# Kernel tuning notes

Hardware: AMD Instinct MI355X
Metric: run time of the kernel (lower is better)

Reference implementation:

```python
import jax, jax.numpy as jnp
import numpy as np

N_LOW = 50000
N_HIGH = 200000
E = 1000000       # number of (i, j, k) triplets from the radius search
K = 27            # 3x3x3 voxel kernel cells
C_IN = 128
C_OUT = 128


def setup_inputs() -> dict:
    key = jax.random.key(0)
    k0, k1, k2, k3, k4, k5 = jax.random.split(key, 6)
    x_low = jax.random.normal(k0, (N_LOW, C_IN), dtype=jnp.float32)
    # PointConv3d weight: one [C_OUT, C_IN] matrix per kernel cell, kaiming-ish scale
    weight = jax.random.normal(k1, (K, C_OUT, C_IN), dtype=jnp.float32) * (1.0 / np.sqrt(C_IN))
    bias = jax.random.normal(k2, (C_OUT,), dtype=jnp.float32) * 0.01
    i_high = jax.random.randint(k3, (E,), 0, N_HIGH, dtype=jnp.int32)
    j_low = jax.random.randint(k4, (E,), 0, N_LOW, dtype=jnp.int32)
    k_cell = jax.random.randint(k5, (E,), 0, K, dtype=jnp.int32)
    return {"x_low": x_low, "weight": weight, "bias": bias,
            "i_high": i_high, "j_low": j_low, "k": k_cell, "n_high": N_HIGH}


def reference(x_low, weight, bias, i_high, j_low, k, n_high):
    # Sparse point convolution: out[i] += weight[k] @ x_low[j], then + bias.
    # Efficient form: transform every low-res point by all K kernel matrices once
    # (dense GEMM), then gather the (j, k) entry per triplet and scatter-add by i.
    y = jnp.einsum('nc,koc->nko', x_low, weight)       # [N_low, K, C_out]
    msg = y[j_low, k]                                  # [E, C_out] gather
    out = jnp.zeros((n_high, weight.shape[1]), dtype=x_low.dtype)
    out = out.at[i_high].add(msg)                      # scatter-add to high-res points
    return out + bias
```

## Files before the change

kernel.cpp:

```cpp
#include <hip/hip_runtime.h>

typedef _Float16 half8 __attribute__((ext_vector_type(8)));
typedef _Float16 half4v __attribute__((ext_vector_type(4)));
typedef _Float16 half2v __attribute__((ext_vector_type(2)));
typedef float f32x4 __attribute__((ext_vector_type(4)));
typedef float f32x2 __attribute__((ext_vector_type(2)));

#define CAP 32
#define OVF_MAX 4096


__global__ void init_bias(float* __restrict__ out, const float* __restrict__ bias, int n4) {
    int i = blockIdx.x * blockDim.x + threadIdx.x;
    if (i >= n4) return;
    reinterpret_cast<float4*>(out)[i] = reinterpret_cast<const float4*>(bias)[i & 31];
}

__global__ __launch_bounds__(256) void cvt_mask(
    const float* __restrict__ x, const float* __restrict__ w,
    const float* __restrict__ bias,
    _Float16* __restrict__ Xh, _Float16* __restrict__ Wh,
    float* __restrict__ biasPerm, _Float16* __restrict__ Yz,
    const int* __restrict__ ih, const int* __restrict__ jl,
    const int* __restrict__ kc,
    unsigned char* __restrict__ maskB,
    int* __restrict__ counts, int* __restrict__ bucket,
    int* __restrict__ ovf_cnt, int* __restrict__ ovf_list,
    int Mpad, int xv4, int xt4, int w4, int E, int eg) {
    int i = blockIdx.x * blockDim.x + threadIdx.x;
    if (i < xt4) {
        float4 v = (i < xv4) ? reinterpret_cast<const float4*>(x)[i]
                             : make_float4(0.f, 0.f, 0.f, 0.f);
        half4v h; h[0]=(_Float16)v.x; h[1]=(_Float16)v.y; h[2]=(_Float16)v.z; h[3]=(_Float16)v.w;
        reinterpret_cast<half4v*>(Xh)[i] = h;
    } else if (i < xt4 + w4) {
        int j = i - xt4;
        float4 v = reinterpret_cast<const float4*>(w)[j];
        half4v h; h[0]=(_Float16)v.x; h[1]=(_Float16)v.y; h[2]=(_Float16)v.z; h[3]=(_Float16)v.w;
        reinterpret_cast<half4v*>(Wh)[j] = h;
    } else if (i < xt4 + w4 + 32) {
        int j2 = i - xt4 - w4;
        int wn = j2 >> 4, mrow = j2 & 15;
        float4 v;
        v.x = bias[wn * 64 + 0 * 16 + mrow];
        v.y = bias[wn * 64 + 1 * 16 + mrow];
        v.z = bias[wn * 64 + 2 * 16 + mrow];
        v.w = bias[wn * 64 + 3 * 16 + mrow];
        reinterpret_cast<float4*>(biasPerm)[j2] = v;
    } else if (i < xt4 + w4 + 48) {
        int t = i - xt4 - w4 - 32;
        reinterpret_cast<int4*>(Yz)[t] = make_int4(0, 0, 0, 0);
    } else {
        int e = i - (xt4 + w4 + 48);
        if (e < E) {
            int j = jl[e], kk = kc[e];
            maskB[(size_t)kk * Mpad + j] = 1;
            if (e >= eg) {
                int ii = ih[e];
                int off = (kk * Mpad + j) * 128;
                int pos = atomicAdd(&counts[ii], 1);
                if (pos < CAP) {
                    bucket[(size_t)ii * CAP + pos] = off;
                } else {
                    int o = atomicAdd(ovf_cnt, 1);
                    if (o < OVF_MAX) { ovf_list[2 * o] = ii; ovf_list[2 * o + 1] = off; }
                }
            }
        }
    }
}

__global__ __launch_bounds__(256, 3) void gemm_xw(
    const _Float16* __restrict__ Xh,
    const _Float16* __restrict__ Wh,
    _Float16* __restrict__ Y,
    const unsigned char* __restrict__ maskB,
    int Mpad, int KD,
    const int* __restrict__ ih, const int* __restrict__ jl,
    const int* __restrict__ kc,
    int* __restrict__ counts, int* __restrict__ bucket,
    int* __restrict__ ovf_cnt, int* __restrict__ ovf_list, int eg) {
    __shared__ ushort sA[64 * 128];
    __shared__ ushort sB[128 * 128];
    const int tid = threadIdx.x;

    const int nwg = gridDim.x;
    const int bid = blockIdx.x;
    const int q = nwg >> 3, r = nwg & 7;
    const int xcd = bid & 7, idx = bid >> 3;
    const int wg = (xcd < r) ? xcd * (q + 1) + idx
                             : r * (q + 1) + (xcd - r) * q + idx;
    const int mtile = wg / KD;
    const int ky = wg - mtile * KD;
    const int m0 = mtile * 64;
    const int kc0 = ky * 3;

    const ushort* Ag = (const ushort*)Xh + (size_t)m0 * 128;
#pragma unroll
    for (int it = 0; it < 4; ++it) {
        int p = it * 256 + tid;
        int row = p >> 4, cpos = p & 15;
        int csrc = cpos ^ (row & 15);
        __builtin_amdgcn_global_load_lds(
            (const __attribute__((address_space(1))) void*)(Ag + row * 128 + csrc * 8),
            (__attribute__((address_space(3))) void*)(&sA[row * 128 + cpos * 8]), 16, 0, 0);
    }
    {
        const ushort* Bg = (const ushort*)Wh + (size_t)kc0 * 128 * 128;
#pragma unroll
        for (int it = 0; it < 8; ++it) {
            int p = it * 256 + tid;
            int row = p >> 4, cpos = p & 15;
            int csrc = cpos ^ (row & 15);
            __builtin_amdgcn_global_load_lds(
                (const __attribute__((address_space(1))) void*)(Bg + row * 128 + csrc * 8),
                (__attribute__((address_space(3))) void*)(&sB[row * 128 + cpos * 8]), 16, 0, 0);
        }
    }
    __builtin_amdgcn_sched_barrier(0);

    const bool hasE = (bid * 256) < eg;
    int i0 = 0, off0 = 0, pos0 = CAP;
    if (hasE) {
        int e = bid * 256 + tid;
        i0 = ih[e];
        off0 = (kc[e] * Mpad + jl[e]) * 128;
        pos0 = atomicAdd(&counts[i0], 1);
        __builtin_amdgcn_sched_barrier(0);
        asm volatile("s_waitcnt vmcnt(4)" ::: "memory");
    } else {
        __builtin_amdgcn_sched_barrier(0);
        asm volatile("s_waitcnt vmcnt(0)" ::: "memory");
    }
    __builtin_amdgcn_sched_barrier(0);
    __builtin_amdgcn_s_barrier();
    __builtin_amdgcn_sched_barrier(0);

    const int lane = tid & 63;
    const int wid = tid >> 6;
    const int wm = wid & 1, wn = wid >> 1;
    const int mrow = lane & 15;
    const int g = lane >> 4;

    for (int kk = 0; kk < 3; ++kk) {
        f32x4 acc[2][4] = {};
#pragma unroll
        for (int kb = 0; kb < 4; ++kb) {
            half8 af[2], bf[4];
            const int cpos8 = ((kb * 4 + g) ^ mrow) * 8;
#pragma unroll
            for (int t = 0; t < 2; ++t) {
                int ra = wm * 32 + t * 16 + mrow;
                af[t] = *reinterpret_cast<const half8*>(&sA[ra * 128 + cpos8]);
            }
#pragma unroll
            for (int t = 0; t < 4; ++t) {
                int rb = wn * 64 + t * 16 + mrow;
                bf[t] = *reinterpret_cast<const half8*>(&sB[rb * 128 + cpos8]);
            }
#pragma unroll
            for (int mt = 0; mt < 2; ++mt)
#pragma unroll
                for (int nt = 0; nt < 4; ++nt)
                    acc[mt][nt] = __builtin_amdgcn_mfma_f32_16x16x32_f16(
                        af[mt], bf[nt], acc[mt][nt], 0, 0, 0);
        }
        if (kk < 2) {
            __builtin_amdgcn_s_barrier();
            __builtin_amdgcn_sched_barrier(0);
            const ushort* Bg = (const ushort*)Wh + (size_t)(kc0 + kk + 1) * 128 * 128;
#pragma unroll
            for (int it = 0; it < 8; ++it) {
                int p = it * 256 + tid;
                int row = p >> 4, cpos = p & 15;
                int csrc = cpos ^ (row & 15);
                __builtin_amdgcn_global_load_lds(
                    (const __attribute__((address_space(1))) void*)(Bg + row * 128 + csrc * 8),
                    (__attribute__((address_space(3))) void*)(&sB[row * 128 + cpos * 8]), 16, 0, 0);
            }
            __builtin_amdgcn_sched_barrier(0);
        }
        if (kk == 0 && hasE) {
            if (pos0 < CAP) {
                bucket[(size_t)i0 * CAP + pos0] = off0;
            } else {
                int o = atomicAdd(ovf_cnt, 1);
                if (o < OVF_MAX) { ovf_list[2 * o] = i0; ovf_list[2 * o + 1] = off0; }
            }
        }
        const unsigned char* mBp = maskB + (size_t)(kc0 + kk) * Mpad + m0 + wm * 32;
        _Float16* Yt = Y + ((size_t)(kc0 + kk) * Mpad + m0) * 128 + wn * 64 + mrow * 4;
#pragma unroll
        for (int mt = 0; mt < 2; ++mt) {
            unsigned mw = *reinterpret_cast<const unsigned*>(mBp + mt * 16 + g * 4);
            if (mw) {
#pragma unroll
                for (int r = 0; r < 4; ++r) {
                    if ((mw >> (8 * r)) & 0xFFu) {
                        int row = wm * 32 + mt * 16 + g * 4 + r;
                        half4v hv;
#pragma unroll
                        for (int nt = 0; nt < 4; ++nt) hv[nt] = (_Float16)acc[mt][nt][r];
                        __builtin_nontemporal_store(
                            hv, reinterpret_cast<half4v*>(Yt + (size_t)row * 128));
                    }
                }
            }
        }
        __builtin_amdgcn_sched_barrier(0);
        if (kk == 0) {
            if (hasE) { asm volatile("s_waitcnt vmcnt(9)" ::: "memory"); }
            else      { asm volatile("s_waitcnt vmcnt(8)" ::: "memory"); }
            __builtin_amdgcn_sched_barrier(0);
            __builtin_amdgcn_s_barrier();
            __builtin_amdgcn_sched_barrier(0);
        } else if (kk == 1) {
            asm volatile("s_waitcnt vmcnt(8)" ::: "memory");
            __builtin_amdgcn_sched_barrier(0);
            __builtin_amdgcn_s_barrier();
            __builtin_amdgcn_sched_barrier(0);
        }
    }
}

__global__ __launch_bounds__(256) void gather_out(
    const _Float16* __restrict__ Y, const int* __restrict__ counts,
    const int* __restrict__ bucket, const float* __restrict__ biasPerm,
    float* __restrict__ out, int Nhigh, int zoff) {
    int wave = (blockIdx.x * blockDim.x + threadIdx.x) >> 6;
    int lane = threadIdx.x & 63;
    int p = lane >> 4;
    int sub = lane & 15;
    int i = wave * 4 + p;
    bool act = i < Nhigh;
    int iC = act ? i : 0;
    int nb = counts[iC];
    if (nb > CAP) nb = CAP;
    const int* bk = bucket + (size_t)iC * CAP;
    int offsA = bk[sub];
    int offsB = bk[sub + 16];
    float4 b0 = reinterpret_cast<const float4*>(biasPerm)[sub * 2];
    float4 b1 = reinterpret_cast<const float4*>(biasPerm)[sub * 2 + 1];
    float acc[8] = {b0.x, b0.y, b0.z, b0.w, b1.x, b1.y, b1.z, b1.w};

    int nmax = nb;
    nmax = max(nmax, __shfl_xor(nmax, 16));
    nmax = max(nmax, __shfl_xor(nmax, 32));

    for (int e0 = 0; e0 < nmax; e0 += 8) {
#pragma unroll
        for (int u = 0; u < 8; ++u) {
            int e = e0 + u;
            int off = (e < 16) ? __shfl(offsA, p * 16 + (e & 15))
                               : __shfl(offsB, p * 16 + (e & 15));
            bool valid = act && (e < nb);
            off = valid ? off : zoff;
            half8 h = *reinterpret_cast<const half8*>(Y + (size_t)off + sub * 8);
#pragma unroll
            for (int t = 0; t < 8; ++t) acc[t] += (float)h[t];
        }
    }
    if (act) {
        float* op = out + (size_t)i * 128;
        int obase = (sub >> 3) * 64 + (sub & 7) * 2;
#pragma unroll
        for (int b = 0; b < 4; ++b) {
            f32x2 v; v[0] = acc[b]; v[1] = acc[b + 4];
            __builtin_nontemporal_store(
                v, reinterpret_cast<f32x2*>(op + obase + 16 * b));
        }
    }
}

__global__ void apply_overflow(const int* __restrict__ ovf_cnt, const int* __restrict__ ovf_list,
                               const _Float16* __restrict__ Y, float* __restrict__ out) {
    int n = *ovf_cnt;
    if (n > OVF_MAX) n = OVF_MAX;
    int lane = threadIdx.x & 63;
    int w = threadIdx.x >> 6;
    int o0p = 2 * lane, o1p = 2 * lane + 1;
    int o0 = (o0p >> 6) * 64 + (o0p & 3) * 16 + ((o0p >> 2) & 15);
    int o1 = (o1p >> 6) * 64 + (o1p & 3) * 16 + ((o1p >> 2) & 15);
    for (int o = w; o < n; o += 4) {
        int i = ovf_list[2 * o], off = ovf_list[2 * o + 1];
        half2v h = *reinterpret_cast<const half2v*>(Y + (size_t)off + lane * 2);
        float* dst = out + (size_t)i * 128;
        unsafeAtomicAdd(dst + o0, (float)h[0]);
        unsafeAtomicAdd(dst + o1, (float)h[1]);
    }
}

__global__ void fallback_edge(const float* __restrict__ x, const float* __restrict__ w,
                              const int* __restrict__ ih, const int* __restrict__ jl,
                              const int* __restrict__ kc, float* __restrict__ out, int E) {
    int e = blockIdx.x;
    if (e >= E) return;
    int lane = threadIdx.x;
    int i = ih[e], j = jl[e], k = kc[e];
    const float* xr = x + (size_t)j * 128;
    const float* wk = w + (size_t)k * 128 * 128;
    float s0 = 0.f, s1 = 0.f;
    for (int c = 0; c < 128; ++c) {
        float xv = xr[c];
        s0 += wk[(size_t)lane * 128 + c] * xv;
        s1 += wk[(size_t)(lane + 64) * 128 + c] * xv;
    }
    unsafeAtomicAdd(&out[(size_t)i * 128 + lane], s0);
    unsafeAtomicAdd(&out[(size_t)i * 128 + 64 + lane], s1);
}

extern "C" void kernel_launch(void* const* d_in, const int* in_sizes, int n_in,
                              void* d_out, int out_size, void* d_ws, size_t ws_size,
                              hipStream_t stream) {
    const float* x    = (const float*)d_in[0];
    const float* w    = (const float*)d_in[1];
    const float* bias = (const float*)d_in[2];
    const int*   ih   = (const int*)d_in[3];
    const int*   jl   = (const int*)d_in[4];
    const int*   kc   = (const int*)d_in[5];
    float* out = (float*)d_out;

    const int C = 128;
    const int Nlow = in_sizes[0] / C;
    const int K = in_sizes[1] / (C * C);
    const int E = in_sizes[3];
    const int Nhigh = out_size / C;

    const int mtiles = (Nlow + 63) / 64;
    const int Mpad = mtiles * 64;

    size_t off = 0;
    auto alloc = [&](size_t bytes) { size_t o = off; off = (off + bytes + 255) & ~(size_t)255; return o; };
    size_t xh_off   = alloc((size_t)Mpad * C * 2);
    size_t wh_off   = alloc((size_t)K * C * C * 2);
    size_t bp_off   = alloc((size_t)C * 4);
    size_t cnt_off  = alloc(((size_t)Nhigh + 1) * 4 + (size_t)Mpad * K);
    size_t ovl_off  = alloc((size_t)OVF_MAX * 2 * 4);
    size_t bkt_off  = alloc((size_t)Nhigh * CAP * 4);
    size_t y_off    = alloc(((size_t)K * Mpad * C + C) * 2);
    size_t need_sort = off;

    _Float16* Xh = (_Float16*)((char*)d_ws + xh_off);
    _Float16* Wh = (_Float16*)((char*)d_ws + wh_off);
    float* biasPerm = (float*)((char*)d_ws + bp_off);
    int* counts  = (int*)((char*)d_ws + cnt_off);
    int* ovf_cnt = counts + Nhigh;
    unsigned char* maskB = (unsigned char*)(counts + Nhigh + 1);
    int* ovf_lst = (int*)((char*)d_ws + ovl_off);
    int* bucket  = (int*)((char*)d_ws + bkt_off);
    _Float16* Y  = (_Float16*)((char*)d_ws + y_off);
    const int zoff = K * Mpad * C;

    if (ws_size >= need_sort && (K % 3) == 0) {
        int xv4 = Nlow * C / 4, xt4 = Mpad * C / 4;
        int w4 = K * C * C / 4;
        int KD = K / 3;
        int nwg = mtiles * KD;
        long long cap256 = (long long)nwg * 256;
        int eg = (E < cap256) ? (E & ~255) : (int)cap256;

        size_t nzb = ((size_t)Nhigh + 1) * 4 + (size_t)Mpad * K;
        hipMemsetAsync(counts, 0, nzb, stream);

        int totalCvt = xt4 + w4 + 48 + E;
        cvt_mask<<<(totalCvt + 255) / 256, 256, 0, stream>>>(
            x, w, bias, Xh, Wh, biasPerm, Y + (size_t)zoff,
            ih, jl, kc, maskB, counts, bucket, ovf_cnt, ovf_lst,
            Mpad, xv4, xt4, w4, E, eg);

        gemm_xw<<<nwg, 256, 0, stream>>>(
            Xh, Wh, Y, maskB, Mpad, KD,
            ih, jl, kc, counts, bucket, ovf_cnt, ovf_lst, eg);

        gather_out<<<(Nhigh + 15) / 16, 256, 0, stream>>>(
            Y, counts, bucket, biasPerm, out, Nhigh, zoff);
        apply_overflow<<<1, 256, 0, stream>>>(ovf_cnt, ovf_lst, Y, out);
    } else {
        int n4out = out_size / 4;
        init_bias<<<(n4out + 255) / 256, 256, 0, stream>>>(out, bias, n4out);
        fallback_edge<<<E, 64, 0, stream>>>(x, w, ih, jl, kc, out, E);
    }
}
```

Baseline: 323.3 us.

## Compact GEMM output rows via mask prefix scan and move all bucketing into GEMM

Adds a two-pass prefix scan over the (k,j) usage mask so the GEMM writes only rows that are actually referenced, packed contiguously into Y, and bucket entries store the compacted row index. All edge bucketing now happens inside the GEMM kernel, and cvt_mask only builds the mask. The intent is to shrink the Y footprint so the gather pass reads a denser, more cache-friendly array. In exchange it adds two small kernel launches and an extra index lookup per edge, drops the nontemporal stores, and takes the fallback path when the edge count exceeds the GEMM thread capacity.

```diff
diff --git a/kernel.cpp b/kernel.cpp
--- a/kernel.cpp
+++ b/kernel.cpp
@@ -21,12 +21,9 @@
     const float* __restrict__ bias,
     _Float16* __restrict__ Xh, _Float16* __restrict__ Wh,
     float* __restrict__ biasPerm, _Float16* __restrict__ Yz,
-    const int* __restrict__ ih, const int* __restrict__ jl,
-    const int* __restrict__ kc,
+    const int* __restrict__ jl, const int* __restrict__ kc,
     unsigned char* __restrict__ maskB,
-    int* __restrict__ counts, int* __restrict__ bucket,
-    int* __restrict__ ovf_cnt, int* __restrict__ ovf_list,
-    int Mpad, int xv4, int xt4, int w4, int E, int eg) {
+    int Mpad, int xv4, int xt4, int w4, int E) {
     int i = blockIdx.x * blockDim.x + threadIdx.x;
     if (i < xt4) {
         float4 v = (i < xv4) ? reinterpret_cast<const float4*>(x)[i]
@@ -52,20 +49,68 @@
         reinterpret_cast<int4*>(Yz)[t] = make_int4(0, 0, 0, 0);
     } else {
         int e = i - (xt4 + w4 + 48);
-        if (e < E) {
-            int j = jl[e], kk = kc[e];
-            maskB[(size_t)kk * Mpad + j] = 1;
-            if (e >= eg) {
-                int ii = ih[e];
-                int off = (kk * Mpad + j) * 128;
-                int pos = atomicAdd(&counts[ii], 1);
-                if (pos < CAP) {
-                    bucket[(size_t)ii * CAP + pos] = off;
-                } else {
-                    int o = atomicAdd(ovf_cnt, 1);
-                    if (o < OVF_MAX) { ovf_list[2 * o] = ii; ovf_list[2 * o + 1] = off; }
-                }
-            }
+        if (e < E) maskB[(size_t)kc[e] * Mpad + jl[e]] = 1;
+    }
+}
+
+__global__ __launch_bounds__(256) void scan_sums(
+    const unsigned* __restrict__ m4, int n4, int* __restrict__ bsums) {
+    int base = blockIdx.x * 1024 + threadIdx.x * 4;
+    int s = 0;
+#pragma unroll
+    for (int t = 0; t < 4; ++t) {
+        int idx = base + t;
+        if (idx < n4) s += __popc(m4[idx]);
+    }
+#pragma unroll
+    for (int o = 32; o; o >>= 1) s += __shfl_xor(s, o);
+    __shared__ int ws[4];
+    if ((threadIdx.x & 63) == 0) ws[threadIdx.x >> 6] = s;
+    __syncthreads();
+    if (threadIdx.x == 0) bsums[blockIdx.x] = ws[0] + ws[1] + ws[2] + ws[3];
+}
+
+__global__ __launch_bounds__(256) void scan_write(
+    const unsigned* __restrict__ m4, int n4,
+    const int* __restrict__ bsums, int* __restrict__ cidx) {
+    const int tid = threadIdx.x, b = blockIdx.x;
+    int acc = 0;
+    for (int i = tid; i < b; i += 256) acc += bsums[i];
+#pragma unroll
+    for (int o = 32; o; o >>= 1) acc += __shfl_xor(acc, o);
+    __shared__ int ws[4];
+    __shared__ int tsum[256];
+    if ((tid & 63) == 0) ws[tid >> 6] = acc;
+    __syncthreads();
+    const int blockOff = ws[0] + ws[1] + ws[2] + ws[3];
+    int base = b * 1024 + tid * 4;
+    unsigned v[4]; int ts = 0;
+#pragma unroll
+    for (int t = 0; t < 4; ++t) {
+        int idx = base + t;
+        v[t] = (idx < n4) ? m4[idx] : 0u;
+        ts += __popc(v[t]);
+    }
+    tsum[tid] = ts;
+    __syncthreads();
+    for (int o = 1; o < 256; o <<= 1) {
+        int y = (tid >= o) ? tsum[tid - o] : 0;
+        __syncthreads();
+        tsum[tid] += y;
+        __syncthreads();
+    }
+    int run = blockOff + tsum[tid] - ts;
+#pragma unroll
+    for (int t = 0; t < 4; ++t) {
+        int idx = base + t;
+        if (idx < n4) {
+            unsigned wv = v[t];
+            int4 o4;
+            o4.x = run; run += (wv & 1u);
+            o4.y = run; run += ((wv >> 8) & 1u);
+            o4.z = run; run += ((wv >> 16) & 1u);
+            o4.w = run; run += ((wv >> 24) & 1u);
+            reinterpret_cast<int4*>(cidx)[idx] = o4;
         }
     }
 }
@@ -75,11 +120,12 @@
     const _Float16* __restrict__ Wh,
     _Float16* __restrict__ Y,
     const unsigned char* __restrict__ maskB,
+    const int* __restrict__ cidx,
     int Mpad, int KD,
     const int* __restrict__ ih, const int* __restrict__ jl,
     const int* __restrict__ kc,
     int* __restrict__ counts, int* __restrict__ bucket,
-    int* __restrict__ ovf_cnt, int* __restrict__ ovf_list, int eg) {
+    int* __restrict__ ovf_cnt, int* __restrict__ ovf_list, int E) {
     __shared__ ushort sA[64 * 128];
     __shared__ ushort sB[128 * 128];
     const int tid = threadIdx.x;
@@ -95,6 +141,22 @@
     const int m0 = mtile * 64;
     const int kc0 = ky * 3;
 
+    const int lane = tid & 63;
+    const int wid = tid >> 6;
+    const int wm = wid & 1, wn = wid >> 1;
+    const int mrow = lane & 15;
+    const int g = lane >> 4;
+
+    const bool anyE = (bid * 256) < E;
+    const bool full = (bid * 256 + 256) <= E;
+
+    int i0 = 0, ej = 0, ek = 0;
+    if (anyE) {
+        int e = bid * 256 + tid;
+        if (e < E) { i0 = ih[e]; ej = jl[e]; ek = kc[e]; }
+    }
+    __builtin_amdgcn_sched_barrier(0);
+
     const ushort* Ag = (const ushort*)Xh + (size_t)m0 * 128;
 #pragma unroll
     for (int it = 0; it < 4; ++it) {
@@ -119,15 +181,25 @@
     }
     __builtin_amdgcn_sched_barrier(0);
 
-    const bool hasE = (bid * 256) < eg;
-    int i0 = 0, off0 = 0, pos0 = CAP;
-    if (hasE) {
+    unsigned char mb0, mb1, mb2; int cb0, cb1, cb2;
+    {
+        const unsigned char* mp = maskB + (size_t)kc0 * Mpad + m0 + lane;
+        mb0 = mp[0]; mb1 = mp[Mpad]; mb2 = mp[2 * Mpad];
+        const int* cp = cidx + (size_t)kc0 * Mpad + m0;
+        cb0 = cp[0]; cb1 = cp[Mpad]; cb2 = cp[2 * Mpad];
+    }
+    __builtin_amdgcn_sched_barrier(0);
+
+    int off0 = 0, pos0 = CAP;
+    if (anyE) {
         int e = bid * 256 + tid;
-        i0 = ih[e];
-        off0 = (kc[e] * Mpad + jl[e]) * 128;
-        pos0 = atomicAdd(&counts[i0], 1);
+        if (e < E) {
+            off0 = cidx[(size_t)ek * Mpad + ej] * 128;
+            pos0 = atomicAdd(&counts[i0], 1);
+        }
         __builtin_amdgcn_sched_barrier(0);
-        asm volatile("s_waitcnt vmcnt(4)" ::: "memory");
+        if (full) { asm volatile("s_waitcnt vmcnt(2)" ::: "memory"); }
+        else      { asm volatile("s_waitcnt vmcnt(0)" ::: "memory"); }
     } else {
         __builtin_amdgcn_sched_barrier(0);
         asm volatile("s_waitcnt vmcnt(0)" ::: "memory");
@@ -136,12 +208,7 @@
     __builtin_amdgcn_s_barrier();
     __builtin_amdgcn_sched_barrier(0);
 
-    const int lane = tid & 63;
-    const int wid = tid >> 6;
-    const int wm = wid & 1, wn = wid >> 1;
-    const int mrow = lane & 15;
-    const int g = lane >> 4;
-
+#pragma unroll
     for (int kk = 0; kk < 3; ++kk) {
         f32x4 acc[2][4] = {};
 #pragma unroll
@@ -167,6 +234,18 @@
         }
         if (kk < 2) {
             __builtin_amdgcn_s_barrier();
+            __builtin_amdgcn_sched_barrier(0);
+            if (kk == 0 && anyE) {
+                int e = bid * 256 + tid;
+                if (e < E) {
+                    if (pos0 < CAP) {
+                        bucket[(size_t)i0 * CAP + pos0] = off0;
+                    } else {
+                        int o = atomicAdd(ovf_cnt, 1);
+                        if (o < OVF_MAX) { ovf_list[2 * o] = i0; ovf_list[2 * o + 1] = off0; }
+                    }
+                }
+            }
             __builtin_amdgcn_sched_barrier(0);
             const ushort* Bg = (const ushort*)Wh + (size_t)(kc0 + kk + 1) * 128 * 128;
 #pragma unroll
@@ -180,42 +259,29 @@
             }
             __builtin_amdgcn_sched_barrier(0);
         }
-        if (kk == 0 && hasE) {
-            if (pos0 < CAP) {
-                bucket[(size_t)i0 * CAP + pos0] = off0;
-            } else {
-                int o = atomicAdd(ovf_cnt, 1);
-                if (o < OVF_MAX) { ovf_list[2 * o] = i0; ovf_list[2 * o + 1] = off0; }
-            }
-        }
-        const unsigned char* mBp = maskB + (size_t)(kc0 + kk) * Mpad + m0 + wm * 32;
-        _Float16* Yt = Y + ((size_t)(kc0 + kk) * Mpad + m0) * 128 + wn * 64 + mrow * 4;
-#pragma unroll
-        for (int mt = 0; mt < 2; ++mt) {
-            unsigned mw = *reinterpret_cast<const unsigned*>(mBp + mt * 16 + g * 4);
-            if (mw) {
-#pragma unroll
-                for (int r = 0; r < 4; ++r) {
-                    if ((mw >> (8 * r)) & 0xFFu) {
-                        int row = wm * 32 + mt * 16 + g * 4 + r;
+        {
+            unsigned char mbk = (kk == 0) ? mb0 : (kk == 1) ? mb1 : mb2;
+            int cbk = (kk == 0) ? cb0 : (kk == 1) ? cb1 : cb2;
+            unsigned long long um = __ballot(mbk != 0);
+            const int colOff = wn * 64 + mrow * 4;
+#pragma unroll
+            for (int mt = 0; mt < 2; ++mt)
+#pragma unroll
+                for (int rr = 0; rr < 4; ++rr) {
+                    int t = wm * 32 + mt * 16 + g * 4 + rr;
+                    if ((um >> t) & 1ull) {
+                        int crow = cbk + __popcll(um & ((1ull << t) - 1ull));
                         half4v hv;
 #pragma unroll
-                        for (int nt = 0; nt < 4; ++nt) hv[nt] = (_Float16)acc[mt][nt][r];
-                        __builtin_nontemporal_store(
-                            hv, reinterpret_cast<half4v*>(Yt + (size_t)row * 128));
+                        for (int nt = 0; nt < 4; ++nt) hv[nt] = (_Float16)acc[mt][nt][rr];
+                        *reinterpret_cast<half4v*>(Y + (size_t)crow * 128 + colOff) = hv;
                     }
                 }
-            }
         }
         __builtin_amdgcn_sched_barrier(0);
-        if (kk == 0) {
-            if (hasE) { asm volatile("s_waitcnt vmcnt(9)" ::: "memory"); }
-            else      { asm volatile("s_waitcnt vmcnt(8)" ::: "memory"); }
-            __builtin_amdgcn_sched_barrier(0);
-            __builtin_amdgcn_s_barrier();
-            __builtin_amdgcn_sched_barrier(0);
-        } else if (kk == 1) {
-            asm volatile("s_waitcnt vmcnt(8)" ::: "memory");
+        if (kk < 2) {
+            if (full) { asm volatile("s_waitcnt vmcnt(8)" ::: "memory"); }
+            else      { asm volatile("s_waitcnt vmcnt(0)" ::: "memory"); }
             __builtin_amdgcn_sched_barrier(0);
             __builtin_amdgcn_s_barrier();
             __builtin_amdgcn_sched_barrier(0);
@@ -328,16 +394,21 @@
 
     const int mtiles = (Nlow + 63) / 64;
     const int Mpad = mtiles * 64;
+    const int NC = Mpad * K;
+    const int nc4 = NC / 4;
+    const int nbScan = (nc4 + 1023) / 1024;
 
     size_t off = 0;
     auto alloc = [&](size_t bytes) { size_t o = off; off = (off + bytes + 255) & ~(size_t)255; return o; };
     size_t xh_off   = alloc((size_t)Mpad * C * 2);
     size_t wh_off   = alloc((size_t)K * C * C * 2);
     size_t bp_off   = alloc((size_t)C * 4);
-    size_t cnt_off  = alloc(((size_t)Nhigh + 1) * 4 + (size_t)Mpad * K);
+    size_t cnt_off  = alloc(((size_t)Nhigh + 1) * 4 + (size_t)NC);
+    size_t cix_off  = alloc((size_t)NC * 4);
+    size_t bs_off   = alloc((size_t)nbScan * 4);
     size_t ovl_off  = alloc((size_t)OVF_MAX * 2 * 4);
     size_t bkt_off  = alloc((size_t)Nhigh * CAP * 4);
-    size_t y_off    = alloc(((size_t)K * Mpad * C + C) * 2);
+    size_t y_off    = alloc(((size_t)NC * C + C) * 2);
     size_t need_sort = off;
 
     _Float16* Xh = (_Float16*)((char*)d_ws + xh_off);
@@ -346,31 +417,35 @@
     int* counts  = (int*)((char*)d_ws + cnt_off);
     int* ovf_cnt = counts + Nhigh;
     unsigned char* maskB = (unsigned char*)(counts + Nhigh + 1);
+    int* cidx    = (int*)((char*)d_ws + cix_off);
+    int* bsums   = (int*)((char*)d_ws + bs_off);
     int* ovf_lst = (int*)((char*)d_ws + ovl_off);
     int* bucket  = (int*)((char*)d_ws + bkt_off);
     _Float16* Y  = (_Float16*)((char*)d_ws + y_off);
-    const int zoff = K * Mpad * C;
-
-    if (ws_size >= need_sort && (K % 3) == 0) {
+    const int zoff = NC * C;
+
+    int KD = K / 3;
+    int nwg = mtiles * KD;
+    bool edgesFit = (long long)E <= (long long)nwg * 256;
+
+    if (ws_size >= need_sort && (K % 3) == 0 && edgesFit) {
         int xv4 = Nlow * C / 4, xt4 = Mpad * C / 4;
         int w4 = K * C * C / 4;
-        int KD = K / 3;
-        int nwg = mtiles * KD;
-        long long cap256 = (long long)nwg * 256;
-        int eg = (E < cap256) ? (E & ~255) : (int)cap256;
-
-        size_t nzb = ((size_t)Nhigh + 1) * 4 + (size_t)Mpad * K;
+
+        size_t nzb = ((size_t)Nhigh + 1) * 4 + (size_t)NC;
         hipMemsetAsync(counts, 0, nzb, stream);
 
         int totalCvt = xt4 + w4 + 48 + E;
         cvt_mask<<<(totalCvt + 255) / 256, 256, 0, stream>>>(
             x, w, bias, Xh, Wh, biasPerm, Y + (size_t)zoff,
-            ih, jl, kc, maskB, counts, bucket, ovf_cnt, ovf_lst,
-            Mpad, xv4, xt4, w4, E, eg);
+            jl, kc, maskB, Mpad, xv4, xt4, w4, E);
+
+        scan_sums<<<nbScan, 256, 0, stream>>>((const unsigned*)maskB, nc4, bsums);
+        scan_write<<<nbScan, 256, 0, stream>>>((const unsigned*)maskB, nc4, bsums, cidx);
 
         gemm_xw<<<nwg, 256, 0, stream>>>(
-            Xh, Wh, Y, maskB, Mpad, KD,
-            ih, jl, kc, counts, bucket, ovf_cnt, ovf_lst, eg);
+            Xh, Wh, Y, maskB, cidx, Mpad, KD,
+            ih, jl, kc, counts, bucket, ovf_cnt, ovf_lst, E);
 
         gather_out<<<(Nhigh + 15) / 16, 256, 0, stream>>>(
             Y, counts, bucket, biasPerm, out, Nhigh, zoff);
```

Result: slower. 340.6 us (+5.3%).
